# Kernel tuning notes

Hardware: AMD Instinct MI355X
Metric: run time of the kernel (lower is better)

Reference implementation:

```python
import jax, jax.numpy as jnp
import numpy as np

NEG_SLOPE = 0.2


def setup_inputs() -> dict:
    key = jax.random.key(0)
    k1, k2, k3, k4, k5, k6 = jax.random.split(key, 6)
    N, E, IN, OUT = 100000, 1600000, 256, 32
    feat = jax.random.normal(k1, (N, IN), dtype=jnp.float32)
    W = jax.random.normal(k2, (IN, OUT), dtype=jnp.float32) * (1.0 / np.sqrt(IN))
    attn_l = jax.random.normal(k3, (OUT,), dtype=jnp.float32) * 0.1
    attn_r = jax.random.normal(k4, (OUT,), dtype=jnp.float32) * 0.1
    bias = jnp.zeros((OUT,), dtype=jnp.float32)
    src = jax.random.randint(k5, (E,), 0, N, dtype=jnp.int32)
    dst = jax.random.randint(k6, (E,), 0, N, dtype=jnp.int32)
    return {"feat": feat, "W": W, "attn_l": attn_l, "attn_r": attn_r,
            "bias": bias, "src": src, "dst": dst}


def reference(feat, W, attn_l, attn_r, bias, src, dst):
    N = feat.shape[0]
    # dense projection: [N, in] @ [in, out] -> [N, out]
    h = feat @ W
    el = h @ attn_l  # [N]
    er = h @ attn_r  # [N]
    # per-edge raw score: el[u] + er[v] for edge u->v
    e = el[src] + er[dst]  # [E]
    e = jnp.where(e > 0, e, NEG_SLOPE * e)  # leaky relu
    # edge softmax grouped by destination node (numerically stable)
    m = jax.ops.segment_max(e, dst, num_segments=N)  # [N], -inf for isolated nodes
    m = jax.lax.stop_gradient(m)
    ex = jnp.exp(e - m[dst])  # [E]
    denom = jax.ops.segment_sum(ex, dst, num_segments=N)  # [N]
    alpha = ex / denom[dst]  # [E]
    # weighted aggregation (sparse SpMM): sum_{u->v} alpha_uv * h[u]
    rst = jax.ops.segment_sum(h[src] * alpha[:, None], dst, num_segments=N)  # [N, out]
    return rst + bias
```

## Files before the change

kernel.cpp:

```cpp
#include <hip/hip_runtime.h>
#include <hip/hip_bf16.h>
#include <math.h>

#define NEG_SLOPE 0.2f
#define BUCK_BITS 5
#define BUCK_NODES 32
#define CAP 800
#define SRC_MASK 0x1FFFFFF
#define NBUK_MAX 3200

#define CBITS 8
#define CNODES 256
#define CAPC 4672
#define NC_MAX 400
#define NBIN 256
#define NGEMM 256

typedef __bf16 bf16x8 __attribute__((ext_vector_type(8)));
typedef __bf16 bf16x4 __attribute__((ext_vector_type(4)));
typedef float  f32x4  __attribute__((ext_vector_type(4)));

__global__ void prep(const float* __restrict__ W, __bf16* __restrict__ Whi,
                     unsigned int* __restrict__ fcur,
                     unsigned int* __restrict__ ccur) {
    int idx = blockIdx.x * blockDim.x + threadIdx.x;
    if (idx < NBUK_MAX) fcur[idx] = 0u;
    if (idx < NC_MAX)   ccur[idx] = 0u;
    if (idx >= 8192) return;
    int j = idx & 7, lane = (idx >> 3) & 63, nt = (idx >> 9) & 1, kt = idx >> 10;
    int q = lane >> 4, c = lane & 15;
    int k = kt * 32 + q * 8 + j;
    int n = nt * 16 + c;
    Whi[idx] = (__bf16)W[k * 32 + n];
}

__global__ __launch_bounds__(256) void gemm_bin(const float* __restrict__ feat,
                                                const __bf16* __restrict__ Whi,
                                                const float* __restrict__ attn_l,
                                                const float* __restrict__ attn_r,
                                                const int* __restrict__ src,
                                                const int* __restrict__ dst,
                                                __bf16* __restrict__ hb,
                                                float* __restrict__ el,
                                                float* __restrict__ er,
                                                unsigned int* __restrict__ ccur,
                                                unsigned int* __restrict__ cbin,
                                                int N, int Ntiles, int E, int NC) {
    union SM {
        struct { bf16x8 whi[1024]; float stage[4][2][1024]; } g;
        struct { unsigned int hist[NC_MAX]; unsigned int cbase[NC_MAX]; } b;
    };
    __shared__ SM sm;

    int bid = blockIdx.x;
    int tid = threadIdx.x;
    int role = bid & 1, gid = bid >> 1;

    if (role == 1) {
        unsigned int* hist  = sm.b.hist;
        unsigned int* cbase = sm.b.cbase;
        int batch = (((E + NBIN - 1) / NBIN) + 3) & ~3;
        int b0 = gid * batch;
        int b1 = min(b0 + batch, E);
        int nv = (b0 < b1) ? ((b1 - b0) >> 2) : 0;
        const int4* d4 = (const int4*)(dst + b0);
        const int4* s4 = (const int4*)(src + b0);
        for (int i = tid; i < NC; i += 256) hist[i] = 0;
        __syncthreads();
        for (int i = tid; i < nv; i += 256) {
            int4 dd = d4[i];
#pragma unroll
            for (int j = 0; j < 4; j++)
                atomicAdd(&hist[((unsigned)(&dd.x)[j]) >> CBITS], 1u);
        }
        __syncthreads();
        for (int i = tid; i < NC; i += 256) {
            unsigned c = hist[i];
            cbase[i] = c ? atomicAdd(&ccur[i], c) : 0u;
            hist[i] = 0;
        }
        __syncthreads();
        for (int i = tid; i < nv; i += 256) {
            int4 dd = d4[i];
            int4 ss = s4[i];
#pragma unroll
            for (int j = 0; j < 4; j++) {
                int d = (&dd.x)[j];
                int s = (&ss.x)[j];
                unsigned cb = ((unsigned)d) >> CBITS;
                unsigned r = atomicAdd(&hist[cb], 1u);
                unsigned pos = cbase[cb] + r;
                if (pos < CAPC)
                    cbin[(size_t)cb * CAPC + pos] =
                        ((unsigned)(d & (CNODES - 1)) << 17) | (unsigned)s;
            }
        }
        return;
    }

    for (int i = tid; i < 1024; i += 256) sm.g.whi[i] = ((const bf16x8*)Whi)[i];
    __syncthreads();

    int wv   = tid >> 6;
    int lane = tid & 63;
    int cc = lane & 15, qd = lane >> 4;
    int swz = (cc & 7) << 4;

    int gw = gid * 4 + wv;
    int nt = (Ntiles - gw + 1023) >> 10;
    int Q  = 4 * nt;

    float* buf0 = &sm.g.stage[wv][0][0];
    float* buf1 = &sm.g.stage[wv][1][0];

    auto stage_q = [&](int q) {
        int qc = q < Q ? q : Q - 1;
        int t  = gw + ((qc >> 2) << 10);
        int kq = qc & 3;
        float* lb = (q & 1) ? buf1 : buf0;
#pragma unroll
        for (int j = 0; j < 4; j++) {
            int r = 4 * j + (lane >> 4);
            int grow = t * 16 + r;
            if (grow >= N) grow = N - 1;
            int seg = ((lane & 15) * 16) ^ ((r & 7) << 4);
            const char* sp = (const char*)feat +
                             ((size_t)grow * 256 + kq * 64) * 4 + seg;
            __builtin_amdgcn_global_load_lds(
                (const __attribute__((address_space(1))) void*)sp,
                (__attribute__((address_space(3))) void*)(lb + j * 256),
                16, 0, 0);
        }
    };

    stage_q(0);
    stage_q(1);

    float alc  = attn_l[cc],      arc  = attn_r[cc];
    float alc2 = attn_l[cc + 16], arc2 = attn_r[cc + 16];

    f32x4 acc0 = {0.f, 0.f, 0.f, 0.f};
    f32x4 acc1 = {0.f, 0.f, 0.f, 0.f};

    for (int i = 0; i < nt; i++) {
#pragma unroll
        for (int kq2 = 0; kq2 < 4; kq2++) {
            int q = i * 4 + kq2;
            asm volatile("s_waitcnt vmcnt(4)" ::: "memory");
            __builtin_amdgcn_sched_barrier(0);
            const char* lb = (const char*)((q & 1) ? buf1 : buf0);
#pragma unroll
            for (int jj = 0; jj < 2; jj++) {
                int kt = kq2 * 2 + jj;
                int so = jj * 128 + qd * 32;
                f32x4 a0 = *(const f32x4*)(lb + cc * 256 + ((so)      ^ swz));
                f32x4 a1 = *(const f32x4*)(lb + cc * 256 + ((so + 16) ^ swz));
                bf16x8 ah, al;
#pragma unroll
                for (int j = 0; j < 4; j++) {
                    __bf16 h0 = (__bf16)a0[j];
                    __bf16 h1 = (__bf16)a1[j];
                    ah[j]     = h0;
                    ah[j + 4] = h1;
                    al[j]     = (__bf16)(a0[j] - (float)h0);
                    al[j + 4] = (__bf16)(a1[j] - (float)h1);
                }
                bf16x8 bh0 = sm.g.whi[(kt * 2 + 0) * 64 + lane];
                bf16x8 bh1 = sm.g.whi[(kt * 2 + 1) * 64 + lane];
                acc0 = __builtin_amdgcn_mfma_f32_16x16x32_bf16(ah, bh0, acc0, 0, 0, 0);
                acc0 = __builtin_amdgcn_mfma_f32_16x16x32_bf16(al, bh0, acc0, 0, 0, 0);
                acc1 = __builtin_amdgcn_mfma_f32_16x16x32_bf16(ah, bh1, acc1, 0, 0, 0);
                acc1 = __builtin_amdgcn_mfma_f32_16x16x32_bf16(al, bh1, acc1, 0, 0, 0);
            }
            if (kq2 == 3) {
                int t = gw + (i << 10);
#pragma unroll
                for (int r = 0; r < 4; r++) {
                    int m = t * 16 + qd * 4 + r;
                    if (m < N) {
                        hb[(size_t)m * 32 + cc]      = (__bf16)acc0[r];
                        hb[(size_t)m * 32 + 16 + cc] = (__bf16)acc1[r];
                    }
                    float pl = acc0[r] * alc + acc1[r] * alc2;
                    float pr = acc0[r] * arc + acc1[r] * arc2;
#pragma unroll
                    for (int off = 8; off >= 1; off >>= 1) {
                        pl += __shfl_xor(pl, off);
                        pr += __shfl_xor(pr, off);
                    }
                    if (cc == 0 && m < N) { el[m] = pl; er[m] = pr; }
                }
                acc0 = (f32x4){0.f, 0.f, 0.f, 0.f};
                acc1 = (f32x4){0.f, 0.f, 0.f, 0.f};
            }
            __builtin_amdgcn_sched_barrier(0);
            stage_q(q + 2);
        }
    }
}

__global__ __launch_bounds__(256) void refine(const unsigned int* __restrict__ ccur,
                                              const unsigned int* __restrict__ cbin,
                                              unsigned int* __restrict__ fcur,
                                              unsigned int* __restrict__ fbin,
                                              int NC) {
    __shared__ unsigned int hist[8];
    __shared__ unsigned int basec[8];
    int blk = blockIdx.x;
    int cb = blk >> 1, seg = blk & 1;
    if (cb >= NC) return;
    int tid = threadIdx.x;
    int cnt = (int)min(ccur[cb], (unsigned)CAPC);
    int lo = (cnt * seg) >> 1;
    int hi = (cnt * (seg + 1)) >> 1;

    if (tid < 8) hist[tid] = 0;
    __syncthreads();
    const unsigned int* cp = cbin + (size_t)cb * CAPC;
    for (int i = lo + tid; i < hi; i += 256)
        atomicAdd(&hist[(cp[i] >> (17 + BUCK_BITS)) & 7], 1u);
    __syncthreads();
    if (tid < 8) {
        unsigned v = hist[tid];
        basec[tid] = v ? atomicAdd(&fcur[cb * 8 + tid], v) : 0u;
        hist[tid] = 0;
    }
    __syncthreads();
    for (int i = lo + tid; i < hi; i += 256) {
        unsigned r = cp[i];
        int fb = (r >> (17 + BUCK_BITS)) & 7;
        unsigned rank = atomicAdd(&hist[fb], 1u);
        unsigned pos = basec[fb] + rank;
        if (pos < CAP)
            fbin[(size_t)(cb * 8 + fb) * CAP + pos] =
                (((r >> 17) & (BUCK_NODES - 1)) << 25) | (r & 0x1FFFFu);
    }
}

__global__ __launch_bounds__(256) void aggregate(const unsigned int* __restrict__ cursor,
                                                 const unsigned int* __restrict__ binned,
                                                 const float* __restrict__ el,
                                                 const float* __restrict__ er,
                                                 const __bf16* __restrict__ hb,
                                                 const float* __restrict__ bias,
                                                 float* __restrict__ out, int N) {
    __shared__ uint2        rw_s[CAP];
    __shared__ unsigned int hist[BUCK_NODES];
    __shared__ int          off_s[BUCK_NODES + 1];
    __shared__ float        den[BUCK_NODES];
    __shared__ float        er_l[BUCK_NODES];

    int buck = blockIdx.x;
    int base = buck << BUCK_BITS;
    int nn = min(BUCK_NODES, N - base);
    int tid = threadIdx.x;

    int cnt = (int)min(cursor[buck], (unsigned)CAP);
    const unsigned int* eb = binned + (size_t)buck * CAP;

    if (tid < BUCK_NODES) {
        hist[tid] = 0;
        den[tid] = 0.f;
        er_l[tid] = (tid < nn) ? er[base + tid] : 0.f;
    }
    __syncthreads();

    unsigned int rl[4];
    int k = 0;
    for (int i = tid; i < cnt; i += 256) {
        unsigned r = eb[i];
        rl[k++] = r;
        atomicAdd(&hist[r >> 25], 1u);
    }
    __syncthreads();

    if (tid < BUCK_NODES) {
        int v = (int)hist[tid];
        int orig = v;
#pragma unroll
        for (int off = 1; off < BUCK_NODES; off <<= 1) {
            int x = __shfl_up(v, off, 64);
            if (tid >= off) v += x;
        }
        off_s[tid] = v - orig;
        if (tid == BUCK_NODES - 1) off_s[BUCK_NODES] = v;
        hist[tid] = (unsigned)(v - orig);
    }
    __syncthreads();

    k = 0;
    for (int i = tid; i < cnt; i += 256) {
        unsigned r = rl[k++];
        int s = r & SRC_MASK;
        int d = r >> 25;
        float e = el[s] + er_l[d];
        e = (e > 0.f) ? e : NEG_SLOPE * e;
        float w = __expf(e);
        unsigned pos = atomicAdd(&hist[d], 1u);
        rw_s[pos] = make_uint2((unsigned)s, __float_as_uint(w));
        atomicAdd(&den[d], w);
    }
    __syncthreads();

    int lane = tid & 63, wv = tid >> 6;
    int oct = lane >> 3, t = lane & 7;
    f32x4 b4 = *(const f32x4*)&bias[t * 4];
    for (int n = wv; n < nn; n += 4) {
        float sm = den[n];
        int s0 = off_s[n], s1 = off_s[n + 1];
        f32x4 acc = {0.f, 0.f, 0.f, 0.f};
#pragma unroll 2
        for (int j = s0 + oct; j < s1; j += 8) {
            uint2 rw = rw_s[j];
            float w = __uint_as_float(rw.y);
            bf16x4 hv = *(const bf16x4*)&hb[(size_t)rw.x * 32 + t * 4];
            acc[0] += w * (float)hv[0];
            acc[1] += w * (float)hv[1];
            acc[2] += w * (float)hv[2];
            acc[3] += w * (float)hv[3];
        }
#pragma unroll
        for (int off = 8; off <= 32; off <<= 1) {
            acc[0] += __shfl_xor(acc[0], off);
            acc[1] += __shfl_xor(acc[1], off);
            acc[2] += __shfl_xor(acc[2], off);
            acc[3] += __shfl_xor(acc[3], off);
        }
        if (lane < 8) {
            f32x4 o;
            if (sm > 0.f) {
                float inv = 1.f / sm;
                o[0] = acc[0] * inv + b4[0];
                o[1] = acc[1] * inv + b4[1];
                o[2] = acc[2] * inv + b4[2];
                o[3] = acc[3] * inv + b4[3];
            } else {
                o = b4;
            }
            *(f32x4*)&out[(size_t)(base + n) * 32 + t * 4] = o;
        }
    }
}

static inline size_t align256(size_t x) { return (x + 255) & ~(size_t)255; }

extern "C" void kernel_launch(void* const* d_in, const int* in_sizes, int n_in,
                              void* d_out, int out_size, void* d_ws, size_t ws_size,
                              hipStream_t stream) {
    const float* feat   = (const float*)d_in[0];
    const float* W      = (const float*)d_in[1];
    const float* attn_l = (const float*)d_in[2];
    const float* attn_r = (const float*)d_in[3];
    const float* bias   = (const float*)d_in[4];
    const int* src = (const int*)d_in[5];
    const int* dst = (const int*)d_in[6];
    float* out = (float*)d_out;

    const int IN = 256;
    int N = in_sizes[0] / IN;
    int E = in_sizes[5];
    (void)n_in; (void)out_size; (void)ws_size;

    int Ntiles = (N + 15) / 16;
    int NBUK = (N + BUCK_NODES - 1) >> BUCK_BITS;
    int NC   = (N + CNODES - 1) >> CBITS;

    char* p = (char*)d_ws;
    __bf16* hb     = (__bf16*)p; p += align256((size_t)N * 32 * 2);
    float* el      = (float*)p; p += align256((size_t)N * 4);
    float* er      = (float*)p; p += align256((size_t)N * 4);
    unsigned int* fcur = (unsigned int*)p; p += align256((size_t)NBUK_MAX * 4);
    unsigned int* ccur = (unsigned int*)p; p += align256((size_t)NC_MAX * 4);
    unsigned int* fbin = (unsigned int*)p; p += align256((size_t)NBUK * CAP * 4);
    unsigned int* cbin = (unsigned int*)p; p += align256((size_t)NC * CAPC * 4);
    __bf16* Whi    = (__bf16*)p; p += align256((size_t)8192 * 2);

    prep<<<33, 256, 0, stream>>>(W, Whi, fcur, ccur);
    gemm_bin<<<NGEMM + NBIN, 256, 0, stream>>>(feat, Whi, attn_l, attn_r,
                                               src, dst, hb, el, er, ccur, cbin,
                                               N, Ntiles, E, NC);
    refine<<<NC * 2, 256, 0, stream>>>(ccur, cbin, fcur, fbin, NC);
    aggregate<<<NBUK, 256, 0, stream>>>(fcur, fbin, el, er, hb, bias, out, N);
}
```

Baseline: 227.1 us.

## Drop refine pass and aggregate directly from 256-node coarse bins

Removes the refine kernel that split each 256-node coarse bin into 32-node fine buckets, and instead has aggregate process a whole coarse bin per 512-thread block with a 256-entry histogram and a multi-wave prefix scan in shared memory. This eliminates one kernel launch plus a full read and write of the edge list through global memory. The cost is far fewer blocks (about 391 instead of about 3125), larger shared memory per block (about 40KB), and possibly lower occupancy and load balance in the aggregation phase.

```diff
diff --git a/kernel.cpp b/kernel.cpp
--- a/kernel.cpp
+++ b/kernel.cpp
@@ -3,11 +3,6 @@
 #include <math.h>
 
 #define NEG_SLOPE 0.2f
-#define BUCK_BITS 5
-#define BUCK_NODES 32
-#define CAP 800
-#define SRC_MASK 0x1FFFFFF
-#define NBUK_MAX 3200
 
 #define CBITS 8
 #define CNODES 256
@@ -21,11 +16,9 @@
 typedef float  f32x4  __attribute__((ext_vector_type(4)));
 
 __global__ void prep(const float* __restrict__ W, __bf16* __restrict__ Whi,
-                     unsigned int* __restrict__ fcur,
                      unsigned int* __restrict__ ccur) {
     int idx = blockIdx.x * blockDim.x + threadIdx.x;
-    if (idx < NBUK_MAX) fcur[idx] = 0u;
-    if (idx < NC_MAX)   ccur[idx] = 0u;
+    if (idx < NC_MAX) ccur[idx] = 0u;
     if (idx >= 8192) return;
     int j = idx & 7, lane = (idx >> 3) & 63, nt = (idx >> 9) & 1, kt = idx >> 10;
     int q = lane >> 4, c = lane & 15;
@@ -199,113 +192,85 @@
     }
 }
 
-__global__ __launch_bounds__(256) void refine(const unsigned int* __restrict__ ccur,
-                                              const unsigned int* __restrict__ cbin,
-                                              unsigned int* __restrict__ fcur,
-                                              unsigned int* __restrict__ fbin,
-                                              int NC) {
-    __shared__ unsigned int hist[8];
-    __shared__ unsigned int basec[8];
-    int blk = blockIdx.x;
-    int cb = blk >> 1, seg = blk & 1;
-    if (cb >= NC) return;
-    int tid = threadIdx.x;
-    int cnt = (int)min(ccur[cb], (unsigned)CAPC);
-    int lo = (cnt * seg) >> 1;
-    int hi = (cnt * (seg + 1)) >> 1;
-
-    if (tid < 8) hist[tid] = 0;
-    __syncthreads();
-    const unsigned int* cp = cbin + (size_t)cb * CAPC;
-    for (int i = lo + tid; i < hi; i += 256)
-        atomicAdd(&hist[(cp[i] >> (17 + BUCK_BITS)) & 7], 1u);
-    __syncthreads();
-    if (tid < 8) {
-        unsigned v = hist[tid];
-        basec[tid] = v ? atomicAdd(&fcur[cb * 8 + tid], v) : 0u;
-        hist[tid] = 0;
-    }
-    __syncthreads();
-    for (int i = lo + tid; i < hi; i += 256) {
-        unsigned r = cp[i];
-        int fb = (r >> (17 + BUCK_BITS)) & 7;
-        unsigned rank = atomicAdd(&hist[fb], 1u);
-        unsigned pos = basec[fb] + rank;
-        if (pos < CAP)
-            fbin[(size_t)(cb * 8 + fb) * CAP + pos] =
-                (((r >> 17) & (BUCK_NODES - 1)) << 25) | (r & 0x1FFFFu);
-    }
-}
-
-__global__ __launch_bounds__(256) void aggregate(const unsigned int* __restrict__ cursor,
-                                                 const unsigned int* __restrict__ binned,
+__global__ __launch_bounds__(512) void aggregate(const unsigned int* __restrict__ ccur,
+                                                 const unsigned int* __restrict__ cbin,
                                                  const float* __restrict__ el,
                                                  const float* __restrict__ er,
                                                  const __bf16* __restrict__ hb,
                                                  const float* __restrict__ bias,
                                                  float* __restrict__ out, int N) {
-    __shared__ uint2        rw_s[CAP];
-    __shared__ unsigned int hist[BUCK_NODES];
-    __shared__ int          off_s[BUCK_NODES + 1];
-    __shared__ float        den[BUCK_NODES];
-    __shared__ float        er_l[BUCK_NODES];
-
-    int buck = blockIdx.x;
-    int base = buck << BUCK_BITS;
-    int nn = min(BUCK_NODES, N - base);
+    __shared__ uint2        rw_s[CAPC];
+    __shared__ unsigned int hist[CNODES];
+    __shared__ int          off_s[CNODES + 1];
+    __shared__ float        den[CNODES];
+    __shared__ float        er_l[CNODES];
+    __shared__ int          wsum[5];
+
+    int cb = blockIdx.x;
+    int base = cb << CBITS;
+    int nn = min(CNODES, N - base);
     int tid = threadIdx.x;
-
-    int cnt = (int)min(cursor[buck], (unsigned)CAP);
-    const unsigned int* eb = binned + (size_t)buck * CAP;
-
-    if (tid < BUCK_NODES) {
+    int lane = tid & 63, wvv = tid >> 6;
+
+    int cnt = (int)min(ccur[cb], (unsigned)CAPC);
+    const unsigned int* cp = cbin + (size_t)cb * CAPC;
+
+    if (tid < CNODES) {
         hist[tid] = 0;
         den[tid] = 0.f;
         er_l[tid] = (tid < nn) ? er[base + tid] : 0.f;
     }
     __syncthreads();
 
-    unsigned int rl[4];
-    int k = 0;
-    for (int i = tid; i < cnt; i += 256) {
-        unsigned r = eb[i];
-        rl[k++] = r;
-        atomicAdd(&hist[r >> 25], 1u);
-    }
-    __syncthreads();
-
-    if (tid < BUCK_NODES) {
-        int v = (int)hist[tid];
-        int orig = v;
-#pragma unroll
-        for (int off = 1; off < BUCK_NODES; off <<= 1) {
+    for (int i = tid; i < cnt; i += 512)
+        atomicAdd(&hist[(cp[i] >> 17) & (CNODES - 1)], 1u);
+    __syncthreads();
+
+    int v = 0, orig = 0;
+    if (tid < CNODES) {
+        v = (int)hist[tid];
+        orig = v;
+#pragma unroll
+        for (int off = 1; off < 64; off <<= 1) {
             int x = __shfl_up(v, off, 64);
-            if (tid >= off) v += x;
-        }
-        off_s[tid] = v - orig;
-        if (tid == BUCK_NODES - 1) off_s[BUCK_NODES] = v;
-        hist[tid] = (unsigned)(v - orig);
-    }
-    __syncthreads();
-
-    k = 0;
-    for (int i = tid; i < cnt; i += 256) {
-        unsigned r = rl[k++];
-        int s = r & SRC_MASK;
-        int d = r >> 25;
-        float e = el[s] + er_l[d];
+            if (lane >= off) v += x;
+        }
+        if (lane == 63) wsum[wvv] = v;
+    }
+    __syncthreads();
+    if (tid == 0) {
+        int s = 0;
+#pragma unroll
+        for (int w = 0; w < 4; w++) { int t = wsum[w]; wsum[w] = s; s += t; }
+        wsum[4] = s;
+    }
+    __syncthreads();
+    if (tid < CNODES) {
+        int off = v - orig + wsum[wvv];
+        off_s[tid] = off;
+        hist[tid] = (unsigned)off;
+        if (tid == CNODES - 1) off_s[CNODES] = wsum[4];
+    }
+    __syncthreads();
+
+    for (int i = tid; i < cnt; i += 512) {
+        unsigned r = cp[i];
+        int s  = (int)(r & 0x1FFFFu);
+        int ln = (int)((r >> 17) & (CNODES - 1));
+        float e = el[s] + er_l[ln];
         e = (e > 0.f) ? e : NEG_SLOPE * e;
         float w = __expf(e);
-        unsigned pos = atomicAdd(&hist[d], 1u);
-        rw_s[pos] = make_uint2((unsigned)s, __float_as_uint(w));
-        atomicAdd(&den[d], w);
-    }
-    __syncthreads();
-
-    int lane = tid & 63, wv = tid >> 6;
+        unsigned pos = atomicAdd(&hist[ln], 1u);
+        if (pos < CAPC) {
+            rw_s[pos] = make_uint2((unsigned)s, __float_as_uint(w));
+            atomicAdd(&den[ln], w);
+        }
+    }
+    __syncthreads();
+
     int oct = lane >> 3, t = lane & 7;
     f32x4 b4 = *(const f32x4*)&bias[t * 4];
-    for (int n = wv; n < nn; n += 4) {
+    for (int n = wvv; n < nn; n += 8) {
         float sm = den[n];
         int s0 = off_s[n], s1 = off_s[n + 1];
         f32x4 acc = {0.f, 0.f, 0.f, 0.f};
@@ -362,23 +327,19 @@
     (void)n_in; (void)out_size; (void)ws_size;
 
     int Ntiles = (N + 15) / 16;
-    int NBUK = (N + BUCK_NODES - 1) >> BUCK_BITS;
     int NC   = (N + CNODES - 1) >> CBITS;
 
     char* p = (char*)d_ws;
     __bf16* hb     = (__bf16*)p; p += align256((size_t)N * 32 * 2);
     float* el      = (float*)p; p += align256((size_t)N * 4);
     float* er      = (float*)p; p += align256((size_t)N * 4);
-    unsigned int* fcur = (unsigned int*)p; p += align256((size_t)NBUK_MAX * 4);
     unsigned int* ccur = (unsigned int*)p; p += align256((size_t)NC_MAX * 4);
-    unsigned int* fbin = (unsigned int*)p; p += align256((size_t)NBUK * CAP * 4);
     unsigned int* cbin = (unsigned int*)p; p += align256((size_t)NC * CAPC * 4);
     __bf16* Whi    = (__bf16*)p; p += align256((size_t)8192 * 2);
 
-    prep<<<33, 256, 0, stream>>>(W, Whi, fcur, ccur);
+    prep<<<33, 256, 0, stream>>>(W, Whi, ccur);
     gemm_bin<<<NGEMM + NBIN, 256, 0, stream>>>(feat, Whi, attn_l, attn_r,
                                                src, dst, hb, el, er, ccur, cbin,
                                                N, Ntiles, E, NC);
-    refine<<<NC * 2, 256, 0, stream>>>(ccur, cbin, fcur, fbin, NC);
-    aggregate<<<NBUK, 256, 0, stream>>>(fcur, fbin, el, er, hb, bias, out, N);
+    aggregate<<<NC, 512, 0, stream>>>(ccur, cbin, el, er, hb, bias, out, N);
 }
```

Measured after the change: 233.7 us. +2.9%, slower.

## Fuse all four stages into one cooperative persistent kernel with grid syncs

Applied to the files above, without the earlier changes.

Merges prep, gemm+binning, refine and aggregate into a single cooperative kernel launched with 512 blocks, using grid-wide syncs between phases and grid-stride loops over refine and aggregate work. This removes three kernel launches and their inter-kernel gaps. In exchange, aggregate now runs over 3125 buckets on only 512 resident blocks, grid syncs add their own cost, and the shared-memory union grows occupancy pressure. SRC_MASK is also narrowed, which is harmless for the packed encoding used.

```diff
diff --git a/kernel.cpp b/kernel.cpp
--- a/kernel.cpp
+++ b/kernel.cpp
@@ -1,12 +1,15 @@
 #include <hip/hip_runtime.h>
 #include <hip/hip_bf16.h>
+#include <hip/hip_cooperative_groups.h>
 #include <math.h>
+
+namespace cg = cooperative_groups;
 
 #define NEG_SLOPE 0.2f
 #define BUCK_BITS 5
 #define BUCK_NODES 32
 #define CAP 800
-#define SRC_MASK 0x1FFFFFF
+#define SRC_MASK 0x1FFFFF
 #define NBUK_MAX 3200
 
 #define CBITS 8
@@ -14,330 +17,312 @@
 #define CAPC 4672
 #define NC_MAX 400
 #define NBIN 256
-#define NGEMM 256
+#define NBLK 512
 
 typedef __bf16 bf16x8 __attribute__((ext_vector_type(8)));
 typedef __bf16 bf16x4 __attribute__((ext_vector_type(4)));
 typedef float  f32x4  __attribute__((ext_vector_type(4)));
 
-__global__ void prep(const float* __restrict__ W, __bf16* __restrict__ Whi,
-                     unsigned int* __restrict__ fcur,
-                     unsigned int* __restrict__ ccur) {
-    int idx = blockIdx.x * blockDim.x + threadIdx.x;
-    if (idx < NBUK_MAX) fcur[idx] = 0u;
-    if (idx < NC_MAX)   ccur[idx] = 0u;
-    if (idx >= 8192) return;
-    int j = idx & 7, lane = (idx >> 3) & 63, nt = (idx >> 9) & 1, kt = idx >> 10;
-    int q = lane >> 4, c = lane & 15;
-    int k = kt * 32 + q * 8 + j;
-    int n = nt * 16 + c;
-    Whi[idx] = (__bf16)W[k * 32 + n];
-}
-
-__global__ __launch_bounds__(256) void gemm_bin(const float* __restrict__ feat,
-                                                const __bf16* __restrict__ Whi,
-                                                const float* __restrict__ attn_l,
-                                                const float* __restrict__ attn_r,
-                                                const int* __restrict__ src,
-                                                const int* __restrict__ dst,
-                                                __bf16* __restrict__ hb,
-                                                float* __restrict__ el,
-                                                float* __restrict__ er,
-                                                unsigned int* __restrict__ ccur,
-                                                unsigned int* __restrict__ cbin,
-                                                int N, int Ntiles, int E, int NC) {
+__global__ __launch_bounds__(256) void fused_all(
+        const float* __restrict__ feat, const float* __restrict__ W,
+        const float* __restrict__ attn_l, const float* __restrict__ attn_r,
+        const float* __restrict__ bias,
+        const int* __restrict__ src, const int* __restrict__ dst,
+        __bf16* __restrict__ hb, float* __restrict__ el,
+        float* __restrict__ er, unsigned int* __restrict__ fcur,
+        unsigned int* __restrict__ ccur, unsigned int* __restrict__ fbin,
+        unsigned int* __restrict__ cbin, __bf16* __restrict__ Whi,
+        float* __restrict__ out,
+        int N, int Ntiles, int E, int NC, int NBUK) {
     union SM {
         struct { bf16x8 whi[1024]; float stage[4][2][1024]; } g;
         struct { unsigned int hist[NC_MAX]; unsigned int cbase[NC_MAX]; } b;
+        struct { unsigned int hist[8]; unsigned int basec[8]; } r;
+        struct { uint2 rw[CAP]; unsigned int hist[BUCK_NODES];
+                 int off[BUCK_NODES + 1]; float den[BUCK_NODES];
+                 float er_l[BUCK_NODES]; } a;
     };
     __shared__ SM sm;
 
+    cg::grid_group grid = cg::this_grid();
     int bid = blockIdx.x;
     int tid = threadIdx.x;
-    int role = bid & 1, gid = bid >> 1;
-
-    if (role == 1) {
-        unsigned int* hist  = sm.b.hist;
-        unsigned int* cbase = sm.b.cbase;
-        int batch = (((E + NBIN - 1) / NBIN) + 3) & ~3;
-        int b0 = gid * batch;
-        int b1 = min(b0 + batch, E);
-        int nv = (b0 < b1) ? ((b1 - b0) >> 2) : 0;
-        const int4* d4 = (const int4*)(dst + b0);
-        const int4* s4 = (const int4*)(src + b0);
-        for (int i = tid; i < NC; i += 256) hist[i] = 0;
-        __syncthreads();
-        for (int i = tid; i < nv; i += 256) {
-            int4 dd = d4[i];
-#pragma unroll
-            for (int j = 0; j < 4; j++)
-                atomicAdd(&hist[((unsigned)(&dd.x)[j]) >> CBITS], 1u);
-        }
-        __syncthreads();
-        for (int i = tid; i < NC; i += 256) {
-            unsigned c = hist[i];
-            cbase[i] = c ? atomicAdd(&ccur[i], c) : 0u;
-            hist[i] = 0;
-        }
-        __syncthreads();
-        for (int i = tid; i < nv; i += 256) {
-            int4 dd = d4[i];
-            int4 ss = s4[i];
-#pragma unroll
-            for (int j = 0; j < 4; j++) {
-                int d = (&dd.x)[j];
-                int s = (&ss.x)[j];
-                unsigned cb = ((unsigned)d) >> CBITS;
-                unsigned r = atomicAdd(&hist[cb], 1u);
-                unsigned pos = cbase[cb] + r;
-                if (pos < CAPC)
-                    cbin[(size_t)cb * CAPC + pos] =
-                        ((unsigned)(d & (CNODES - 1)) << 17) | (unsigned)s;
-            }
-        }
-        return;
+
+    {
+        int idx = bid * 256 + tid;
+        if (idx < NBUK_MAX) fcur[idx] = 0u;
+        if (idx < NC_MAX)   ccur[idx] = 0u;
+        if (idx < 8192) {
+            int j = idx & 7, lane = (idx >> 3) & 63, nt = (idx >> 9) & 1,
+                kt = idx >> 10;
+            int q = lane >> 4, c = lane & 15;
+            Whi[idx] = (__bf16)W[(kt * 32 + q * 8 + j) * 32 + nt * 16 + c];
+        }
     }
-
-    for (int i = tid; i < 1024; i += 256) sm.g.whi[i] = ((const bf16x8*)Whi)[i];
-    __syncthreads();
-
-    int wv   = tid >> 6;
-    int lane = tid & 63;
-    int cc = lane & 15, qd = lane >> 4;
-    int swz = (cc & 7) << 4;
-
-    int gw = gid * 4 + wv;
-    int nt = (Ntiles - gw + 1023) >> 10;
-    int Q  = 4 * nt;
-
-    float* buf0 = &sm.g.stage[wv][0][0];
-    float* buf1 = &sm.g.stage[wv][1][0];
-
-    auto stage_q = [&](int q) {
-        int qc = q < Q ? q : Q - 1;
-        int t  = gw + ((qc >> 2) << 10);
-        int kq = qc & 3;
-        float* lb = (q & 1) ? buf1 : buf0;
-#pragma unroll
-        for (int j = 0; j < 4; j++) {
-            int r = 4 * j + (lane >> 4);
-            int grow = t * 16 + r;
-            if (grow >= N) grow = N - 1;
-            int seg = ((lane & 15) * 16) ^ ((r & 7) << 4);
-            const char* sp = (const char*)feat +
-                             ((size_t)grow * 256 + kq * 64) * 4 + seg;
-            __builtin_amdgcn_global_load_lds(
-                (const __attribute__((address_space(1))) void*)sp,
-                (__attribute__((address_space(3))) void*)(lb + j * 256),
-                16, 0, 0);
-        }
-    };
-
-    stage_q(0);
-    stage_q(1);
-
-    float alc  = attn_l[cc],      arc  = attn_r[cc];
-    float alc2 = attn_l[cc + 16], arc2 = attn_r[cc + 16];
-
-    f32x4 acc0 = {0.f, 0.f, 0.f, 0.f};
-    f32x4 acc1 = {0.f, 0.f, 0.f, 0.f};
-
-    for (int i = 0; i < nt; i++) {
-#pragma unroll
-        for (int kq2 = 0; kq2 < 4; kq2++) {
-            int q = i * 4 + kq2;
-            asm volatile("s_waitcnt vmcnt(4)" ::: "memory");
-            __builtin_amdgcn_sched_barrier(0);
-            const char* lb = (const char*)((q & 1) ? buf1 : buf0);
-#pragma unroll
-            for (int jj = 0; jj < 2; jj++) {
-                int kt = kq2 * 2 + jj;
-                int so = jj * 128 + qd * 32;
-                f32x4 a0 = *(const f32x4*)(lb + cc * 256 + ((so)      ^ swz));
-                f32x4 a1 = *(const f32x4*)(lb + cc * 256 + ((so + 16) ^ swz));
-                bf16x8 ah, al;
+    grid.sync();
+
+    {
+        int role = bid & 1, gid = bid >> 1;
+        if (role == 1) {
+            unsigned int* hist  = sm.b.hist;
+            unsigned int* cbase = sm.b.cbase;
+            int batch = (((E + NBIN - 1) / NBIN) + 3) & ~3;
+            int b0 = gid * batch;
+            int b1 = min(b0 + batch, E);
+            int nv = (b0 < b1) ? ((b1 - b0) >> 2) : 0;
+            const int4* d4 = (const int4*)(dst + b0);
+            const int4* s4 = (const int4*)(src + b0);
+            for (int i = tid; i < NC; i += 256) hist[i] = 0;
+            __syncthreads();
+            for (int i = tid; i < nv; i += 256) {
+                int4 dd = d4[i];
+#pragma unroll
+                for (int j = 0; j < 4; j++)
+                    atomicAdd(&hist[((unsigned)(&dd.x)[j]) >> CBITS], 1u);
+            }
+            __syncthreads();
+            for (int i = tid; i < NC; i += 256) {
+                unsigned c = hist[i];
+                cbase[i] = c ? atomicAdd(&ccur[i], c) : 0u;
+                hist[i] = 0;
+            }
+            __syncthreads();
+            for (int i = tid; i < nv; i += 256) {
+                int4 dd = d4[i];
+                int4 ss = s4[i];
 #pragma unroll
                 for (int j = 0; j < 4; j++) {
-                    __bf16 h0 = (__bf16)a0[j];
-                    __bf16 h1 = (__bf16)a1[j];
-                    ah[j]     = h0;
-                    ah[j + 4] = h1;
-                    al[j]     = (__bf16)(a0[j] - (float)h0);
-                    al[j + 4] = (__bf16)(a1[j] - (float)h1);
+                    int d = (&dd.x)[j];
+                    int s = (&ss.x)[j];
+                    unsigned cb = ((unsigned)d) >> CBITS;
+                    unsigned r = atomicAdd(&hist[cb], 1u);
+                    unsigned pos = cbase[cb] + r;
+                    if (pos < CAPC)
+                        cbin[(size_t)cb * CAPC + pos] =
+                            ((unsigned)(d & (CNODES - 1)) << 17) | (unsigned)s;
                 }
-                bf16x8 bh0 = sm.g.whi[(kt * 2 + 0) * 64 + lane];
-                bf16x8 bh1 = sm.g.whi[(kt * 2 + 1) * 64 + lane];
-                acc0 = __builtin_amdgcn_mfma_f32_16x16x32_bf16(ah, bh0, acc0, 0, 0, 0);
-                acc0 = __builtin_amdgcn_mfma_f32_16x16x32_bf16(al, bh0, acc0, 0, 0, 0);
-                acc1 = __builtin_amdgcn_mfma_f32_16x16x32_bf16(ah, bh1, acc1, 0, 0, 0);
-                acc1 = __builtin_amdgcn_mfma_f32_16x16x32_bf16(al, bh1, acc1, 0, 0, 0);
-            }
-            if (kq2 == 3) {
-                int t = gw + (i << 10);
-#pragma unroll
-                for (int r = 0; r < 4; r++) {
-                    int m = t * 16 + qd * 4 + r;
-                    if (m < N) {
-                        hb[(size_t)m * 32 + cc]      = (__bf16)acc0[r];
-                        hb[(size_t)m * 32 + 16 + cc] = (__bf16)acc1[r];
+            }
+        } else {
+            for (int i = tid; i < 1024; i += 256)
+                sm.g.whi[i] = ((const bf16x8*)Whi)[i];
+            __syncthreads();
+
+            int wv   = tid >> 6;
+            int lane = tid & 63;
+            int cc = lane & 15, qd = lane >> 4;
+            int swz = (cc & 7) << 4;
+            int gw = gid * 4 + wv;
+            int nt = (Ntiles - gw + 1023) >> 10;
+            int Q  = 4 * nt;
+            float* buf0 = &sm.g.stage[wv][0][0];
+            float* buf1 = &sm.g.stage[wv][1][0];
+
+            auto stage_q = [&](int q) {
+                int qc = q < Q ? q : Q - 1;
+                int t  = gw + ((qc >> 2) << 10);
+                int kq = qc & 3;
+                float* lb = (q & 1) ? buf1 : buf0;
+#pragma unroll
+                for (int j = 0; j < 4; j++) {
+                    int r = 4 * j + (lane >> 4);
+                    int grow = t * 16 + r;
+                    if (grow >= N) grow = N - 1;
+                    int seg = ((lane & 15) * 16) ^ ((r & 7) << 4);
+                    const char* sp = (const char*)feat +
+                                     ((size_t)grow * 256 + kq * 64) * 4 + seg;
+                    __builtin_amdgcn_global_load_lds(
+                        (const __attribute__((address_space(1))) void*)sp,
+                        (__attribute__((address_space(3))) void*)(lb + j * 256),
+                        16, 0, 0);
+                }
+            };
+
+            stage_q(0);
+            stage_q(1);
+
+            float alc  = attn_l[cc],      arc  = attn_r[cc];
+            float alc2 = attn_l[cc + 16], arc2 = attn_r[cc + 16];
+            f32x4 acc0 = {0.f, 0.f, 0.f, 0.f};
+            f32x4 acc1 = {0.f, 0.f, 0.f, 0.f};
+
+            for (int i = 0; i < nt; i++) {
+#pragma unroll
+                for (int kq2 = 0; kq2 < 4; kq2++) {
+                    int q = i * 4 + kq2;
+                    asm volatile("s_waitcnt vmcnt(4)" ::: "memory");
+                    __builtin_amdgcn_sched_barrier(0);
+                    const char* lb = (const char*)((q & 1) ? buf1 : buf0);
+#pragma unroll
+                    for (int jj = 0; jj < 2; jj++) {
+                        int kt = kq2 * 2 + jj;
+                        int so = jj * 128 + qd * 32;
+                        f32x4 a0 = *(const f32x4*)(lb + cc * 256 + ((so)      ^ swz));
+                        f32x4 a1 = *(const f32x4*)(lb + cc * 256 + ((so + 16) ^ swz));
+                        bf16x8 ah, al;
+#pragma unroll
+                        for (int j = 0; j < 4; j++) {
+                            __bf16 h0 = (__bf16)a0[j];
+                            __bf16 h1 = (__bf16)a1[j];
+                            ah[j]     = h0;
+                            ah[j + 4] = h1;
+                            al[j]     = (__bf16)(a0[j] - (float)h0);
+                            al[j + 4] = (__bf16)(a1[j] - (float)h1);
+                        }
+                        bf16x8 bh0 = sm.g.whi[(kt * 2 + 0) * 64 + lane];
+                        bf16x8 bh1 = sm.g.whi[(kt * 2 + 1) * 64 + lane];
+                        acc0 = __builtin_amdgcn_mfma_f32_16x16x32_bf16(ah, bh0, acc0, 0, 0, 0);
+                        acc0 = __builtin_amdgcn_mfma_f32_16x16x32_bf16(al, bh0, acc0, 0, 0, 0);
+                        acc1 = __builtin_amdgcn_mfma_f32_16x16x32_bf16(ah, bh1, acc1, 0, 0, 0);
+                        acc1 = __builtin_amdgcn_mfma_f32_16x16x32_bf16(al, bh1, acc1, 0, 0, 0);
                     }
-                    float pl = acc0[r] * alc + acc1[r] * alc2;
-                    float pr = acc0[r] * arc + acc1[r] * arc2;
-#pragma unroll
-                    for (int off = 8; off >= 1; off >>= 1) {
-                        pl += __shfl_xor(pl, off);
-                        pr += __shfl_xor(pr, off);
+                    if (kq2 == 3) {
+                        int t = gw + (i << 10);
+#pragma unroll
+                        for (int r = 0; r < 4; r++) {
+                            int m = t * 16 + qd * 4 + r;
+                            if (m < N) {
+                                hb[(size_t)m * 32 + cc]      = (__bf16)acc0[r];
+                                hb[(size_t)m * 32 + 16 + cc] = (__bf16)acc1[r];
+                            }
+                            float pl = acc0[r] * alc + acc1[r] * alc2;
+                            float pr = acc0[r] * arc + acc1[r] * arc2;
+#pragma unroll
+                            for (int off = 8; off >= 1; off >>= 1) {
+                                pl += __shfl_xor(pl, off);
+                                pr += __shfl_xor(pr, off);
+                            }
+                            if (cc == 0 && m < N) { el[m] = pl; er[m] = pr; }
+                        }
+                        acc0 = (f32x4){0.f, 0.f, 0.f, 0.f};
+                        acc1 = (f32x4){0.f, 0.f, 0.f, 0.f};
                     }
-                    if (cc == 0 && m < N) { el[m] = pl; er[m] = pr; }
+                    __builtin_amdgcn_sched_barrier(0);
+                    stage_q(q + 2);
                 }
-                acc0 = (f32x4){0.f, 0.f, 0.f, 0.f};
-                acc1 = (f32x4){0.f, 0.f, 0.f, 0.f};
-            }
-            __builtin_amdgcn_sched_barrier(0);
-            stage_q(q + 2);
+            }
         }
     }
-}
-
-__global__ __launch_bounds__(256) void refine(const unsigned int* __restrict__ ccur,
-                                              const unsigned int* __restrict__ cbin,
-                                              unsigned int* __restrict__ fcur,
-                                              unsigned int* __restrict__ fbin,
-                                              int NC) {
-    __shared__ unsigned int hist[8];
-    __shared__ unsigned int basec[8];
-    int blk = blockIdx.x;
-    int cb = blk >> 1, seg = blk & 1;
-    if (cb >= NC) return;
-    int tid = threadIdx.x;
-    int cnt = (int)min(ccur[cb], (unsigned)CAPC);
-    int lo = (cnt * seg) >> 1;
-    int hi = (cnt * (seg + 1)) >> 1;
-
-    if (tid < 8) hist[tid] = 0;
-    __syncthreads();
-    const unsigned int* cp = cbin + (size_t)cb * CAPC;
-    for (int i = lo + tid; i < hi; i += 256)
-        atomicAdd(&hist[(cp[i] >> (17 + BUCK_BITS)) & 7], 1u);
-    __syncthreads();
-    if (tid < 8) {
-        unsigned v = hist[tid];
-        basec[tid] = v ? atomicAdd(&fcur[cb * 8 + tid], v) : 0u;
-        hist[tid] = 0;
+    grid.sync();
+
+    for (int u = bid; u < 2 * NC; u += NBLK) {
+        __syncthreads();
+        int cb = u >> 1, seg = u & 1;
+        int cnt = (int)min(ccur[cb], (unsigned)CAPC);
+        int lo = (cnt * seg) >> 1;
+        int hi = (cnt * (seg + 1)) >> 1;
+
+        if (tid < 8) sm.r.hist[tid] = 0;
+        __syncthreads();
+        const unsigned int* cp = cbin + (size_t)cb * CAPC;
+        for (int i = lo + tid; i < hi; i += 256)
+            atomicAdd(&sm.r.hist[(cp[i] >> (17 + BUCK_BITS)) & 7], 1u);
+        __syncthreads();
+        if (tid < 8) {
+            unsigned v = sm.r.hist[tid];
+            sm.r.basec[tid] = v ? atomicAdd(&fcur[cb * 8 + tid], v) : 0u;
+            sm.r.hist[tid] = 0;
+        }
+        __syncthreads();
+        for (int i = lo + tid; i < hi; i += 256) {
+            unsigned r = cp[i];
+            int fb = (r >> (17 + BUCK_BITS)) & 7;
+            unsigned rank = atomicAdd(&sm.r.hist[fb], 1u);
+            unsigned pos = sm.r.basec[fb] + rank;
+            if (pos < CAP)
+                fbin[(size_t)(cb * 8 + fb) * CAP + pos] =
+                    (((r >> 17) & (BUCK_NODES - 1)) << 25) | (r & 0x1FFFFu);
+        }
     }
-    __syncthreads();
-    for (int i = lo + tid; i < hi; i += 256) {
-        unsigned r = cp[i];
-        int fb = (r >> (17 + BUCK_BITS)) & 7;
-        unsigned rank = atomicAdd(&hist[fb], 1u);
-        unsigned pos = basec[fb] + rank;
-        if (pos < CAP)
-            fbin[(size_t)(cb * 8 + fb) * CAP + pos] =
-                (((r >> 17) & (BUCK_NODES - 1)) << 25) | (r & 0x1FFFFu);
-    }
-}
-
-__global__ __launch_bounds__(256) void aggregate(const unsigned int* __restrict__ cursor,
-                                                 const unsigned int* __restrict__ binned,
-                                                 const float* __restrict__ el,
-                                                 const float* __restrict__ er,
-                                                 const __bf16* __restrict__ hb,
-                                                 const float* __restrict__ bias,
-                                                 float* __restrict__ out, int N) {
-    __shared__ uint2        rw_s[CAP];
-    __shared__ unsigned int hist[BUCK_NODES];
-    __shared__ int          off_s[BUCK_NODES + 1];
-    __shared__ float        den[BUCK_NODES];
-    __shared__ float        er_l[BUCK_NODES];
-
-    int buck = blockIdx.x;
-    int base = buck << BUCK_BITS;
-    int nn = min(BUCK_NODES, N - base);
-    int tid = threadIdx.x;
-
-    int cnt = (int)min(cursor[buck], (unsigned)CAP);
-    const unsigned int* eb = binned + (size_t)buck * CAP;
-
-    if (tid < BUCK_NODES) {
-        hist[tid] = 0;
-        den[tid] = 0.f;
-        er_l[tid] = (tid < nn) ? er[base + tid] : 0.f;
-    }
-    __syncthreads();
-
-    unsigned int rl[4];
-    int k = 0;
-    for (int i = tid; i < cnt; i += 256) {
-        unsigned r = eb[i];
-        rl[k++] = r;
-        atomicAdd(&hist[r >> 25], 1u);
-    }
-    __syncthreads();
-
-    if (tid < BUCK_NODES) {
-        int v = (int)hist[tid];
-        int orig = v;
-#pragma unroll
-        for (int off = 1; off < BUCK_NODES; off <<= 1) {
-            int x = __shfl_up(v, off, 64);
-            if (tid >= off) v += x;
-        }
-        off_s[tid] = v - orig;
-        if (tid == BUCK_NODES - 1) off_s[BUCK_NODES] = v;
-        hist[tid] = (unsigned)(v - orig);
-    }
-    __syncthreads();
-
-    k = 0;
-    for (int i = tid; i < cnt; i += 256) {
-        unsigned r = rl[k++];
-        int s = r & SRC_MASK;
-        int d = r >> 25;
-        float e = el[s] + er_l[d];
-        e = (e > 0.f) ? e : NEG_SLOPE * e;
-        float w = __expf(e);
-        unsigned pos = atomicAdd(&hist[d], 1u);
-        rw_s[pos] = make_uint2((unsigned)s, __float_as_uint(w));
-        atomicAdd(&den[d], w);
-    }
-    __syncthreads();
-
-    int lane = tid & 63, wv = tid >> 6;
-    int oct = lane >> 3, t = lane & 7;
-    f32x4 b4 = *(const f32x4*)&bias[t * 4];
-    for (int n = wv; n < nn; n += 4) {
-        float sm = den[n];
-        int s0 = off_s[n], s1 = off_s[n + 1];
-        f32x4 acc = {0.f, 0.f, 0.f, 0.f};
+    grid.sync();
+
+    for (int u = bid; u < NBUK; u += NBLK) {
+        __syncthreads();
+        int base = u << BUCK_BITS;
+        int nn = min(BUCK_NODES, N - base);
+        int cnt = (int)min(fcur[u], (unsigned)CAP);
+        const unsigned int* eb = fbin + (size_t)u * CAP;
+
+        if (tid < BUCK_NODES) {
+            sm.a.hist[tid] = 0;
+            sm.a.den[tid] = 0.f;
+            sm.a.er_l[tid] = (tid < nn) ? er[base + tid] : 0.f;
+        }
+        __syncthreads();
+
+        unsigned int rl[4];
+        int k = 0;
+        for (int i = tid; i < cnt; i += 256) {
+            unsigned r = eb[i];
+            rl[k++] = r;
+            atomicAdd(&sm.a.hist[r >> 25], 1u);
+        }
+        __syncthreads();
+
+        if (tid < BUCK_NODES) {
+            int v = (int)sm.a.hist[tid];
+            int orig = v;
+#pragma unroll
+            for (int off = 1; off < BUCK_NODES; off <<= 1) {
+                int x = __shfl_up(v, off, 64);
+                if (tid >= off) v += x;
+            }
+            sm.a.off[tid] = v - orig;
+            if (tid == BUCK_NODES - 1) sm.a.off[BUCK_NODES] = v;
+            sm.a.hist[tid] = (unsigned)(v - orig);
+        }
+        __syncthreads();
+
+        k = 0;
+        for (int i = tid; i < cnt; i += 256) {
+            unsigned r = rl[k++];
+            int s = r & SRC_MASK;
+            int d = r >> 25;
+            float e = el[s] + sm.a.er_l[d];
+            e = (e > 0.f) ? e : NEG_SLOPE * e;
+            float w = __expf(e);
+            unsigned pos = atomicAdd(&sm.a.hist[d], 1u);
+            sm.a.rw[pos] = make_uint2((unsigned)s, __float_as_uint(w));
+            atomicAdd(&sm.a.den[d], w);
+        }
+        __syncthreads();
+
+        int lane = tid & 63, wv = tid >> 6;
+        int oct = lane >> 3, t = lane & 7;
+        f32x4 b4 = *(const f32x4*)&bias[t * 4];
+        for (int n = wv; n < nn; n += 4) {
+            float smv = sm.a.den[n];
+            int s0 = sm.a.off[n], s1 = sm.a.off[n + 1];
+            f32x4 acc = {0.f, 0.f, 0.f, 0.f};
 #pragma unroll 2
-        for (int j = s0 + oct; j < s1; j += 8) {
-            uint2 rw = rw_s[j];
-            float w = __uint_as_float(rw.y);
-            bf16x4 hv = *(const bf16x4*)&hb[(size_t)rw.x * 32 + t * 4];
-            acc[0] += w * (float)hv[0];
-            acc[1] += w * (float)hv[1];
-            acc[2] += w * (float)hv[2];
-            acc[3] += w * (float)hv[3];
-        }
-#pragma unroll
-        for (int off = 8; off <= 32; off <<= 1) {
-            acc[0] += __shfl_xor(acc[0], off);
-            acc[1] += __shfl_xor(acc[1], off);
-            acc[2] += __shfl_xor(acc[2], off);
-            acc[3] += __shfl_xor(acc[3], off);
-        }
-        if (lane < 8) {
-            f32x4 o;
-            if (sm > 0.f) {
-                float inv = 1.f / sm;
-                o[0] = acc[0] * inv + b4[0];
-                o[1] = acc[1] * inv + b4[1];
-                o[2] = acc[2] * inv + b4[2];
-                o[3] = acc[3] * inv + b4[3];
-            } else {
-                o = b4;
-            }
-            *(f32x4*)&out[(size_t)(base + n) * 32 + t * 4] = o;
+            for (int j = s0 + oct; j < s1; j += 8) {
+                uint2 rw = sm.a.rw[j];
+                float w = __uint_as_float(rw.y);
+                bf16x4 hv = *(const bf16x4*)&hb[(size_t)rw.x * 32 + t * 4];
+                acc[0] += w * (float)hv[0];
+                acc[1] += w * (float)hv[1];
+                acc[2] += w * (float)hv[2];
+                acc[3] += w * (float)hv[3];
+            }
+#pragma unroll
+            for (int off = 8; off <= 32; off <<= 1) {
+                acc[0] += __shfl_xor(acc[0], off);
+                acc[1] += __shfl_xor(acc[1], off);
+                acc[2] += __shfl_xor(acc[2], off);
+                acc[3] += __shfl_xor(acc[3], off);
+            }
+            if (lane < 8) {
+                f32x4 o;
+                if (smv > 0.f) {
+                    float inv = 1.f / smv;
+                    o[0] = acc[0] * inv + b4[0];
+                    o[1] = acc[1] * inv + b4[1];
+                    o[2] = acc[2] * inv + b4[2];
+                    o[3] = acc[3] * inv + b4[3];
+                } else {
+                    o = b4;
+                }
+                *(f32x4*)&out[(size_t)(base + n) * 32 + t * 4] = o;
+            }
         }
     }
 }
@@ -375,10 +360,13 @@
     unsigned int* cbin = (unsigned int*)p; p += align256((size_t)NC * CAPC * 4);
     __bf16* Whi    = (__bf16*)p; p += align256((size_t)8192 * 2);
 
-    prep<<<33, 256, 0, stream>>>(W, Whi, fcur, ccur);
-    gemm_bin<<<NGEMM + NBIN, 256, 0, stream>>>(feat, Whi, attn_l, attn_r,
-                                               src, dst, hb, el, er, ccur, cbin,
-                                               N, Ntiles, E, NC);
-    refine<<<NC * 2, 256, 0, stream>>>(ccur, cbin, fcur, fbin, NC);
-    aggregate<<<NBUK, 256, 0, stream>>>(fcur, fbin, el, er, hb, bias, out, N);
+    void* args[] = {
+        (void*)&feat, (void*)&W, (void*)&attn_l, (void*)&attn_r, (void*)&bias,
+        (void*)&src, (void*)&dst, (void*)&hb, (void*)&el, (void*)&er,
+        (void*)&fcur, (void*)&ccur, (void*)&fbin, (void*)&cbin, (void*)&Whi,
+        (void*)&out, (void*)&N, (void*)&Ntiles, (void*)&E, (void*)&NC,
+        (void*)&NBUK
+    };
+    hipLaunchCooperativeKernel((const void*)fused_all, dim3(NBLK), dim3(256),
+                               args, 0, stream);
 }
```

Result: slower. 450.5 us (+98.4%).
